# Performance work log

Measured on AMD Instinct MI355X. Metric: run time of the kernel, lower is better.

Reference implementation:

```python
import jax, jax.numpy as jnp
import numpy as np

N = 3072      # packed vision tokens (multiple of _BLOCK=128, so no padding needed)
D = 1280      # hidden_size
H = 16        # num_heads
K = 80        # head_dim = D // H
NSEG = 8      # number of packed images/segments


def setup_inputs() -> dict:
    key = jax.random.key(0)
    ks = jax.random.split(key, 8)
    hidden_ND = jax.random.normal(ks[0], (N, D), jnp.float32)
    inner = jnp.sort(jax.random.randint(ks[1], (NSEG - 1,), 1, N)).astype(jnp.int32)
    cu_seqlens = jnp.concatenate([
        jnp.zeros((1,), jnp.int32), inner, jnp.full((1,), N, jnp.int32)])
    theta = jax.random.uniform(ks[2], (N, K), jnp.float32, 0.0, 2.0 * np.pi)
    cos_NK = jnp.cos(theta)
    sin_NK = jnp.sin(theta)
    sd = 1.0 / np.sqrt(D)  # lecun_normal-ish scale
    qkv_w = jax.random.normal(ks[3], (D, 3 * D), jnp.float32) * sd
    qkv_b = jax.random.normal(ks[4], (3 * D,), jnp.float32) * 0.01
    proj_w = jax.random.normal(ks[5], (D, D), jnp.float32) * sd
    proj_b = jax.random.normal(ks[6], (D,), jnp.float32) * 0.01
    return {"hidden_ND": hidden_ND, "cu_seqlens": cu_seqlens,
            "cos_NK": cos_NK, "sin_NK": sin_NK,
            "qkv_w": qkv_w, "qkv_b": qkv_b,
            "proj_w": proj_w, "proj_b": proj_b}


def _rotate_half(x):
    x1, x2 = jnp.split(x, 2, axis=-1)
    return jnp.concatenate([-x2, x1], axis=-1)


def _apply_vision_rope(q_NHK, k_NHK, cos_NK, sin_NK):
    c = cos_NK[:, None, :]  # (N, 1, K) broadcast over heads
    s = sin_NK[:, None, :]
    q = q_NHK * c + _rotate_half(q_NHK) * s
    k = k_NHK * c + _rotate_half(k_NHK) * s
    return q, k


def reference(hidden_ND, cu_seqlens, cos_NK, sin_NK, qkv_w, qkv_b, proj_w, proj_b):
    n = hidden_ND.shape[0]
    scale = K ** (-0.5)
    qkv = (hidden_ND @ qkv_w + qkv_b).reshape(n, 3, H, K)
    q_NHK, k_NHK, v_NHK = qkv[:, 0], qkv[:, 1], qkv[:, 2]
    q_NHK, k_NHK = _apply_vision_rope(q_NHK, k_NHK, cos_NK, sin_NK)

    # segment-boundary mask: token i attends to [k_start[i], k_end[i])
    idx = jnp.arange(n)
    seg = jnp.searchsorted(cu_seqlens[1:], idx, side='right')
    nseg = cu_seqlens.shape[0]
    k_start = cu_seqlens[jnp.minimum(seg, nseg - 2)]
    k_end = cu_seqlens[jnp.minimum(seg + 1, nseg - 1)]
    mask = (idx[None, :] >= k_start[:, None]) & (idx[None, :] < k_end[:, None])  # (Nq, Nk)

    scores = jnp.einsum('nhk,mhk->hnm', q_NHK, k_NHK) * scale  # (H, N, N)
    scores = jnp.where(mask[None], scores, jnp.float32(-1e30))
    probs = jax.nn.softmax(scores, axis=-1)
    attn = jnp.einsum('hnm,mhk->nhk', probs, v_NHK)  # (N, H, K)
    out_ND = attn.reshape(n, H * K) @ proj_w + proj_b
    return out_ND
```

## Files before the change

kernel.cpp:

```cpp
#include <hip/hip_runtime.h>

#define NTOK 3072
#define DM   1280
#define NH   16
#define HD   80
#define HDP  96
#define NSEG 8
#define QKVC 3840

typedef __attribute__((ext_vector_type(4))) float  f32x4;
typedef __attribute__((ext_vector_type(8))) __bf16 bf16x8;
typedef __attribute__((ext_vector_type(8))) unsigned short ushort8;
typedef __attribute__((ext_vector_type(4))) unsigned short ushort4v;

static __device__ __forceinline__ unsigned short f2bf(float f){
  union{float f; unsigned int u;} v; v.f=f;
  unsigned int r = v.u + 0x7fffu + ((v.u>>16)&1u);
  return (unsigned short)(r>>16);
}
static __device__ __forceinline__ float bf2f(unsigned short u){
  union{unsigned int i; float f;} v; v.i = ((unsigned int)u)<<16; return v.f;
}
static __device__ __forceinline__ void gload_lds16(const void* g, void* l){
  __builtin_amdgcn_global_load_lds((const __attribute__((address_space(1))) void*)g,
                                   (__attribute__((address_space(3))) void*)l, 16, 0, 0);
}

__global__ void cast_f32_bf16(const float* __restrict__ src, unsigned short* __restrict__ dst, int n){
  int i = (blockIdx.x*256 + threadIdx.x)*4;
  if (i >= n) return;
  f32x4 v = *reinterpret_cast<const f32x4*>(&src[i]);
  ushort4v o;
  o[0]=f2bf(v[0]); o[1]=f2bf(v[1]); o[2]=f2bf(v[2]); o[3]=f2bf(v[3]);
  *reinterpret_cast<ushort4v*>(&dst[i]) = o;
}

__global__ void transpose_cast(const float* __restrict__ src, unsigned short* __restrict__ dst, int R, int C){
  __shared__ unsigned short tile[32][33];
  int c0 = blockIdx.x*32, r0 = blockIdx.y*32;
  int tx = threadIdx.x, ty = threadIdx.y;
  #pragma unroll
  for (int i=0;i<4;i++){
    int r = r0 + ty + i*8;
    tile[ty+i*8][tx] = f2bf(src[(size_t)r*C + c0 + tx]);
  }
  __syncthreads();
  #pragma unroll
  for (int i=0;i<4;i++){
    int c = c0 + ty + i*8;
    dst[(size_t)c*R + r0 + tx] = tile[tx][ty+i*8];
  }
}

template<int OUT_BF16>
__global__ __launch_bounds__(256) void gemm_bt(
    const unsigned short* __restrict__ A,
    const unsigned short* __restrict__ Bt,
    const float* __restrict__ bias,
    unsigned short* __restrict__ Cb,
    float* __restrict__ Cf,
    int M, int Ncol, int Kd)
{
  __shared__ unsigned short As[128*32];
  __shared__ unsigned short Bs[128*32];
  const int tid  = threadIdx.x;
  const int lane = tid & 63, wave = tid >> 6;
  const int wr = wave >> 1, wc = wave & 1;
  const int bm = blockIdx.y, bn = blockIdx.x;
  const f32x4 vzero = {0.f,0.f,0.f,0.f};

  f32x4 acc[4][4];
  #pragma unroll
  for (int i=0;i<4;i++)
    #pragma unroll
    for (int j=0;j<4;j++) acc[i][j] = vzero;

  const int rsub = lane>>2;
  const int kc   = (lane&3)*8;
  const unsigned short* Ab = A  + (size_t)(bm*128 + wave*32 + rsub)*Kd + kc;
  const unsigned short* Bb = Bt + (size_t)(bn*128 + wave*32 + rsub)*Kd + kc;

  for (int k0=0; k0<Kd; k0+=32){
    __syncthreads();
    #pragma unroll
    for (int i=0;i<2;i++){
      gload_lds16(Ab + (size_t)i*16*Kd + k0, &As[(wave*2+i)*512]);
      gload_lds16(Bb + (size_t)i*16*Kd + k0, &Bs[(wave*2+i)*512]);
    }
    __syncthreads();
    bf16x8 a[4], b[4];
    #pragma unroll
    for (int mf=0; mf<4; mf++)
      a[mf] = *reinterpret_cast<const bf16x8*>(&As[(wr*64 + mf*16 + (lane&15))*32 + ((lane>>4)<<3)]);
    #pragma unroll
    for (int nf=0; nf<4; nf++)
      b[nf] = *reinterpret_cast<const bf16x8*>(&Bs[(wc*64 + nf*16 + (lane&15))*32 + ((lane>>4)<<3)]);
    #pragma unroll
    for (int mf=0; mf<4; mf++)
      #pragma unroll
      for (int nf=0; nf<4; nf++)
        acc[mf][nf] = __builtin_amdgcn_mfma_f32_16x16x32_bf16(a[mf], b[nf], acc[mf][nf], 0,0,0);
  }

  const int crow0 = bm*128 + wr*64;
  const int ccol0 = bn*128 + wc*64;
  #pragma unroll
  for (int nf=0; nf<4; nf++){
    int col = ccol0 + nf*16 + (lane&15);
    float bv = bias[col];
    #pragma unroll
    for (int mf=0; mf<4; mf++){
      #pragma unroll
      for (int r=0;r<4;r++){
        int row = crow0 + mf*16 + ((lane>>4)<<2) + r;
        float v = acc[mf][nf][r] + bv;
        if (OUT_BF16) Cb[(size_t)row*Ncol + col] = f2bf(v);
        else          Cf[(size_t)row*Ncol + col] = v;
      }
    }
  }
}

__global__ void rope_repack(const unsigned short* __restrict__ qkv,
                            const float* __restrict__ cosNK, const float* __restrict__ sinNK,
                            unsigned short* __restrict__ Qr, unsigned short* __restrict__ Kr)
{
  int idx = blockIdx.x*256 + threadIdx.x;
  int k  = idx % HDP;
  int nh = idx / HDP;
  int n  = nh % NTOK;
  int h  = nh / NTOK;
  size_t dsti = (size_t)(h*NTOK + n)*HDP + k;
  if (k >= HD){ Qr[dsti]=0; Kr[dsti]=0; return; }
  float c = cosNK[n*HD + k], s = sinNK[n*HD + k];
  int   kp  = (k < 40) ? (k+40) : (k-40);
  float sgn = (k < 40) ? -1.f : 1.f;
  size_t base = (size_t)n*QKVC + h*HD;
  float q   = bf2f(qkv[base + k]);
  float qp  = bf2f(qkv[base + kp]);
  float kk  = bf2f(qkv[base + DM + k]);
  float kkp = bf2f(qkv[base + DM + kp]);
  Qr[dsti] = f2bf(q*c  + sgn*qp*s);
  Kr[dsti] = f2bf(kk*c + sgn*kkp*s);
}

__global__ __launch_bounds__(256) void attn_kernel(
    const unsigned short* __restrict__ Qr,
    const unsigned short* __restrict__ Kr,
    const unsigned short* __restrict__ qkv,
    const int* __restrict__ cu,
    unsigned short* __restrict__ attn_out)
{
  __shared__ unsigned short Qs[64*HDP];
  __shared__ unsigned short Ks[64*HDP];
  __shared__ unsigned short Vst[HDP*64];
  __shared__ unsigned short Ps[64*64];
  __shared__ int rs[64], re[64];

  const int h   = blockIdx.y;
  const int q0  = blockIdx.x*64;
  const int tid = threadIdx.x;
  const int lane = tid & 63;
  const int wave = tid >> 6;
  const f32x4 vzero = {0.f,0.f,0.f,0.f};

  if (tid < 64){
    int row = q0 + tid;
    int seg = 0;
    #pragma unroll
    for (int j=1;j<NSEG;j++) seg += (cu[j] <= row) ? 1 : 0;
    rs[tid] = cu[seg];
    re[tid] = cu[seg+1];
  }
  {
    const unsigned short* src = Qr + ((size_t)h*NTOK + q0)*HDP;
    #pragma unroll
    for (int i=0;i<3;i++){
      int off = i*2048 + tid*8;
      *reinterpret_cast<ushort8*>(&Qs[off]) = *reinterpret_cast<const ushort8*>(&src[off]);
    }
  }
  __syncthreads();
  int kmin = NTOK, kmax = 0;
  for (int j=0;j<64;j++){
    int a = rs[j]; if (a < kmin) kmin = a;
    int b = re[j]; if (b > kmax) kmax = b;
  }

  f32x4 accO[6];
  #pragma unroll
  for (int i=0;i<6;i++) accO[i] = vzero;
  float m_r[4] = {-1e30f,-1e30f,-1e30f,-1e30f};
  float l_r[4] = {0.f,0.f,0.f,0.f};
  const int row_lds0 = wave*16 + ((lane>>4)<<2);

  for (int kt = (kmin/64)*64; kt < kmax; kt += 64){
    __syncthreads();
    {
      const unsigned short* src = Kr + ((size_t)h*NTOK + kt)*HDP;
      #pragma unroll
      for (int i=0;i<3;i++){
        int off = i*2048 + tid*8;
        *reinterpret_cast<ushort8*>(&Ks[off]) = *reinterpret_cast<const ushort8*>(&src[off]);
      }
    }
    if (tid < 128){
      int r = tid >> 1, cb = (tid & 1)*40;
      const unsigned short* src = qkv + (size_t)(kt + r)*QKVC + 2*DM + h*HD + cb;
      #pragma unroll
      for (int jj=0;jj<5;jj++){
        ushort8 v = *reinterpret_cast<const ushort8*>(&src[jj*8]);
        #pragma unroll
        for (int e=0;e<8;e++) Vst[(cb + jj*8 + e)*64 + r] = v[e];
      }
    } else {
      int t2 = tid - 128;
      #pragma unroll
      for (int e=0;e<8;e++) Vst[80*64 + t2*8 + e] = 0;
    }
    __syncthreads();

    f32x4 accS[4];
    #pragma unroll
    for (int i=0;i<4;i++) accS[i] = vzero;
    #pragma unroll
    for (int ks=0; ks<3; ks++){
      bf16x8 aq = *reinterpret_cast<const bf16x8*>(&Qs[(wave*16 + (lane&15))*HDP + ks*32 + ((lane>>4)<<3)]);
      #pragma unroll
      for (int nf=0;nf<4;nf++){
        bf16x8 bk = *reinterpret_cast<const bf16x8*>(&Ks[(nf*16 + (lane&15))*HDP + ks*32 + ((lane>>4)<<3)]);
        accS[nf] = __builtin_amdgcn_mfma_f32_16x16x32_bf16(aq, bk, accS[nf], 0,0,0);
      }
    }
    const float scale = 0.11180339887498948f;
    #pragma unroll
    for (int r=0;r<4;r++){
      int row_i = row_lds0 + r;
      int rst = rs[row_i], ren = re[row_i];
      float sv[4]; bool ok[4];
      float mx = -1e30f;
      #pragma unroll
      for (int nf=0;nf<4;nf++){
        int kcol = kt + nf*16 + (lane&15);
        ok[nf] = (kcol >= rst) && (kcol < ren);
        sv[nf] = accS[nf][r]*scale;
        if (ok[nf]) mx = fmaxf(mx, sv[nf]);
      }
      #pragma unroll
      for (int d=1; d<16; d<<=1) mx = fmaxf(mx, __shfl_xor(mx, d, 64));
      float mnew  = fmaxf(m_r[r], mx);
      float alpha = __expf(m_r[r] - mnew);
      m_r[r] = mnew;
      float lsum = 0.f;
      #pragma unroll
      for (int nf=0;nf<4;nf++){
        float p = ok[nf] ? __expf(sv[nf] - mnew) : 0.f;
        Ps[row_i*64 + nf*16 + (lane&15)] = f2bf(p);
        lsum += p;
      }
      #pragma unroll
      for (int d=1; d<16; d<<=1) lsum += __shfl_xor(lsum, d, 64);
      l_r[r] = l_r[r]*alpha + lsum;
      #pragma unroll
      for (int cf=0; cf<6; cf++) accO[cf][r] *= alpha;
    }
    #pragma unroll
    for (int ks=0; ks<2; ks++){
      bf16x8 ap = *reinterpret_cast<const bf16x8*>(&Ps[(wave*16 + (lane&15))*64 + ks*32 + ((lane>>4)<<3)]);
      #pragma unroll
      for (int cf=0; cf<6; cf++){
        bf16x8 bv = *reinterpret_cast<const bf16x8*>(&Vst[(cf*16 + (lane&15))*64 + ks*32 + ((lane>>4)<<3)]);
        accO[cf] = __builtin_amdgcn_mfma_f32_16x16x32_bf16(ap, bv, accO[cf], 0,0,0);
      }
    }
  }

  #pragma unroll
  for (int cf=0; cf<5; cf++){
    #pragma unroll
    for (int r=0;r<4;r++){
      int row = q0 + row_lds0 + r;
      int col = h*HD + cf*16 + (lane&15);
      float o = accO[cf][r] / l_r[r];
      attn_out[(size_t)row*DM + col] = f2bf(o);
    }
  }
}

extern "C" void kernel_launch(void* const* d_in, const int* in_sizes, int n_in,
                              void* d_out, int out_size, void* d_ws, size_t ws_size,
                              hipStream_t stream)
{
  const float* hidden = (const float*)d_in[0];
  const int*   cu     = (const int*)  d_in[1];
  const float* cosNK  = (const float*)d_in[2];
  const float* sinNK  = (const float*)d_in[3];
  const float* qkv_w  = (const float*)d_in[4];
  const float* qkv_b  = (const float*)d_in[5];
  const float* proj_w = (const float*)d_in[6];
  const float* proj_b = (const float*)d_in[7];
  float* out = (float*)d_out;

  char* w = (char*)d_ws;
  unsigned short* hid_bf  = (unsigned short*)w;  w += (size_t)NTOK*DM*2;
  unsigned short* qkvwT   = (unsigned short*)w;  w += (size_t)QKVC*DM*2;
  unsigned short* projwT  = (unsigned short*)w;  w += (size_t)DM*DM*2;
  unsigned short* qkv_bf  = (unsigned short*)w;  w += (size_t)NTOK*QKVC*2;
  unsigned short* Qr      = (unsigned short*)w;  w += (size_t)NH*NTOK*HDP*2;
  unsigned short* Kr      = (unsigned short*)w;  w += (size_t)NH*NTOK*HDP*2;
  unsigned short* attn_bf = (unsigned short*)w;  w += (size_t)NTOK*DM*2;

  cast_f32_bf16<<<(NTOK*DM/4 + 255)/256, 256, 0, stream>>>(hidden, hid_bf, NTOK*DM);
  transpose_cast<<<dim3(QKVC/32, DM/32), dim3(32,8), 0, stream>>>(qkv_w, qkvwT, DM, QKVC);
  transpose_cast<<<dim3(DM/32,  DM/32), dim3(32,8), 0, stream>>>(proj_w, projwT, DM, DM);
  gemm_bt<1><<<dim3(QKVC/128, NTOK/128), 256, 0, stream>>>(hid_bf, qkvwT, qkv_b, qkv_bf, nullptr, NTOK, QKVC, DM);
  rope_repack<<<(NH*NTOK*HDP)/256, 256, 0, stream>>>(qkv_bf, cosNK, sinNK, Qr, Kr);
  attn_kernel<<<dim3(NTOK/64, NH), 256, 0, stream>>>(Qr, Kr, qkv_bf, cu, attn_bf);
  gemm_bt<0><<<dim3(DM/128, NTOK/128), 256, 0, stream>>>(attn_bf, projwT, proj_b, nullptr, out, NTOK, DM, DM);
}
```

Measured before the change: 266.4 us.

## Restructure attention with 128-wide KV tiles, pre-transposed V and async LDS loads

The attention kernel now processes 128 keys per iteration instead of 64. A new transpose_v kernel writes V once into a head-major, token-contiguous layout, which replaces the per-block scalar transpose into shared memory. Q, K and V tiles are loaded with global_load_lds. The K/Q row stride is padded to 104, and the P and V tiles use XOR swizzles to cut LDS bank conflicts; the padded fifth output fragment is also dropped. This trades an extra kernel launch and more LDS per block (which may lower occupancy) for fewer loop iterations, cheaper staging and less per-tile overhead.

```diff
diff --git a/kernel.cpp b/kernel.cpp
--- a/kernel.cpp
+++ b/kernel.cpp
@@ -4,7 +4,8 @@
 #define DM   1280
 #define NH   16
 #define HD   80
-#define HDP  96
+#define HDS  104
+#define KVB  128
 #define NSEG 8
 #define QKVC 3840
 
@@ -49,6 +50,24 @@
   for (int i=0;i<4;i++){
     int c = c0 + ty + i*8;
     dst[(size_t)c*R + r0 + tx] = tile[tx][ty+i*8];
+  }
+}
+
+__global__ void transpose_v(const unsigned short* __restrict__ qkv, unsigned short* __restrict__ Vt){
+  __shared__ unsigned short tile[32][33];
+  int n0 = blockIdx.x*32, d0 = blockIdx.y*32, h = blockIdx.z;
+  int tx = threadIdx.x, ty = threadIdx.y;
+  #pragma unroll
+  for (int i=0;i<4;i++){
+    int n = n0 + ty + i*8;
+    int d = d0 + tx;
+    tile[ty+i*8][tx] = (d < HD) ? qkv[(size_t)n*QKVC + 2*DM + h*HD + d] : (unsigned short)0;
+  }
+  __syncthreads();
+  #pragma unroll
+  for (int i=0;i<4;i++){
+    int d = d0 + ty + i*8;
+    if (d < HD) Vt[((size_t)h*HD + d)*NTOK + n0 + tx] = tile[tx][ty+i*8];
   }
 }
 
@@ -126,11 +145,12 @@
                             unsigned short* __restrict__ Qr, unsigned short* __restrict__ Kr)
 {
   int idx = blockIdx.x*256 + threadIdx.x;
-  int k  = idx % HDP;
-  int nh = idx / HDP;
+  if (idx >= NH*NTOK*HDS) return;
+  int k  = idx % HDS;
+  int nh = idx / HDS;
   int n  = nh % NTOK;
   int h  = nh / NTOK;
-  size_t dsti = (size_t)(h*NTOK + n)*HDP + k;
+  size_t dsti = (size_t)(h*NTOK + n)*HDS + k;
   if (k >= HD){ Qr[dsti]=0; Kr[dsti]=0; return; }
   float c = cosNK[n*HD + k], s = sinNK[n*HD + k];
   int   kp  = (k < 40) ? (k+40) : (k-40);
@@ -147,101 +167,90 @@
 __global__ __launch_bounds__(256) void attn_kernel(
     const unsigned short* __restrict__ Qr,
     const unsigned short* __restrict__ Kr,
-    const unsigned short* __restrict__ qkv,
+    const unsigned short* __restrict__ Vt,
     const int* __restrict__ cu,
     unsigned short* __restrict__ attn_out)
 {
-  __shared__ unsigned short Qs[64*HDP];
-  __shared__ unsigned short Ks[64*HDP];
-  __shared__ unsigned short Vst[HDP*64];
-  __shared__ unsigned short Ps[64*64];
+  __shared__ unsigned short Qs[64*HDS];
+  __shared__ unsigned short Ks[KVB*HDS];
+  __shared__ unsigned short Vs[HD*KVB];
+  __shared__ unsigned short Ps[64*KVB];
   __shared__ int rs[64], re[64];
 
   const int h   = blockIdx.y;
   const int q0  = blockIdx.x*64;
   const int tid = threadIdx.x;
-  const int lane = tid & 63;
-  const int wave = tid >> 6;
+  const int lane = tid & 63, wave = tid >> 6;
+  const int l16 = lane & 15, g16 = lane >> 4;
   const f32x4 vzero = {0.f,0.f,0.f,0.f};
 
   if (tid < 64){
-    int row = q0 + tid;
-    int seg = 0;
+    int row = q0 + tid, seg = 0;
     #pragma unroll
     for (int j=1;j<NSEG;j++) seg += (cu[j] <= row) ? 1 : 0;
-    rs[tid] = cu[seg];
-    re[tid] = cu[seg+1];
+    rs[tid] = cu[seg]; re[tid] = cu[seg+1];
   }
   {
-    const unsigned short* src = Qr + ((size_t)h*NTOK + q0)*HDP;
-    #pragma unroll
-    for (int i=0;i<3;i++){
-      int off = i*2048 + tid*8;
-      *reinterpret_cast<ushort8*>(&Qs[off]) = *reinterpret_cast<const ushort8*>(&src[off]);
+    const char* src = (const char*)(Qr + (size_t)(h*NTOK + q0)*HDS);
+    #pragma unroll
+    for (int i=0;i<4;i++){
+      int t = tid + i*256;
+      if (t < 832) gload_lds16(src + (size_t)t*16, (char*)Qs + (size_t)t*16);
     }
   }
   __syncthreads();
-  int kmin = NTOK, kmax = 0;
-  for (int j=0;j<64;j++){
-    int a = rs[j]; if (a < kmin) kmin = a;
-    int b = re[j]; if (b > kmax) kmax = b;
-  }
-
-  f32x4 accO[6];
-  #pragma unroll
-  for (int i=0;i<6;i++) accO[i] = vzero;
+  const int kmin = rs[0], kmax = re[63];
+
+  f32x4 accO[5];
+  #pragma unroll
+  for (int i=0;i<5;i++) accO[i] = vzero;
   float m_r[4] = {-1e30f,-1e30f,-1e30f,-1e30f};
   float l_r[4] = {0.f,0.f,0.f,0.f};
-  const int row_lds0 = wave*16 + ((lane>>4)<<2);
-
-  for (int kt = (kmin/64)*64; kt < kmax; kt += 64){
+  const float scale = 0.11180339887498948f;
+
+  for (int kt = (kmin/KVB)*KVB; kt < kmax; kt += KVB){
     __syncthreads();
     {
-      const unsigned short* src = Kr + ((size_t)h*NTOK + kt)*HDP;
-      #pragma unroll
-      for (int i=0;i<3;i++){
-        int off = i*2048 + tid*8;
-        *reinterpret_cast<ushort8*>(&Ks[off]) = *reinterpret_cast<const ushort8*>(&src[off]);
-      }
-    }
-    if (tid < 128){
-      int r = tid >> 1, cb = (tid & 1)*40;
-      const unsigned short* src = qkv + (size_t)(kt + r)*QKVC + 2*DM + h*HD + cb;
-      #pragma unroll
-      for (int jj=0;jj<5;jj++){
-        ushort8 v = *reinterpret_cast<const ushort8*>(&src[jj*8]);
-        #pragma unroll
-        for (int e=0;e<8;e++) Vst[(cb + jj*8 + e)*64 + r] = v[e];
-      }
-    } else {
-      int t2 = tid - 128;
-      #pragma unroll
-      for (int e=0;e<8;e++) Vst[80*64 + t2*8 + e] = 0;
+      const char* src = (const char*)(Kr + (size_t)(h*NTOK + kt)*HDS);
+      #pragma unroll
+      for (int i=0;i<7;i++){
+        int t = tid + i*256;
+        if (t < 1664) gload_lds16(src + (size_t)t*16, (char*)Ks + (size_t)t*16);
+      }
+    }
+    {
+      #pragma unroll
+      for (int i=0;i<5;i++){
+        int t = tid + i*256;
+        int row = t >> 4;
+        int ch  = (t & 15) ^ (row & 7);
+        const unsigned short* src = Vt + ((size_t)h*HD + row)*NTOK + kt + ch*8;
+        gload_lds16(src, (char*)Vs + (size_t)t*16);
+      }
     }
     __syncthreads();
 
-    f32x4 accS[4];
-    #pragma unroll
-    for (int i=0;i<4;i++) accS[i] = vzero;
+    f32x4 accS[8];
+    #pragma unroll
+    for (int i=0;i<8;i++) accS[i] = vzero;
     #pragma unroll
     for (int ks=0; ks<3; ks++){
-      bf16x8 aq = *reinterpret_cast<const bf16x8*>(&Qs[(wave*16 + (lane&15))*HDP + ks*32 + ((lane>>4)<<3)]);
-      #pragma unroll
-      for (int nf=0;nf<4;nf++){
-        bf16x8 bk = *reinterpret_cast<const bf16x8*>(&Ks[(nf*16 + (lane&15))*HDP + ks*32 + ((lane>>4)<<3)]);
+      bf16x8 aq = *reinterpret_cast<const bf16x8*>((const char*)Qs + (wave*16 + l16)*208 + ks*64 + g16*16);
+      #pragma unroll
+      for (int nf=0;nf<8;nf++){
+        bf16x8 bk = *reinterpret_cast<const bf16x8*>((const char*)Ks + (nf*16 + l16)*208 + ks*64 + g16*16);
         accS[nf] = __builtin_amdgcn_mfma_f32_16x16x32_bf16(aq, bk, accS[nf], 0,0,0);
       }
     }
-    const float scale = 0.11180339887498948f;
     #pragma unroll
     for (int r=0;r<4;r++){
-      int row_i = row_lds0 + r;
-      int rst = rs[row_i], ren = re[row_i];
-      float sv[4]; bool ok[4];
+      const int row_i = wave*16 + g16*4 + r;
+      const int rst = rs[row_i], ren = re[row_i];
+      float sv[8]; bool ok[8];
       float mx = -1e30f;
       #pragma unroll
-      for (int nf=0;nf<4;nf++){
-        int kcol = kt + nf*16 + (lane&15);
+      for (int nf=0;nf<8;nf++){
+        int kcol = kt + nf*16 + l16;
         ok[nf] = (kcol >= rst) && (kcol < ren);
         sv[nf] = accS[nf][r]*scale;
         if (ok[nf]) mx = fmaxf(mx, sv[nf]);
@@ -253,23 +262,26 @@
       m_r[r] = mnew;
       float lsum = 0.f;
       #pragma unroll
-      for (int nf=0;nf<4;nf++){
+      for (int nf=0;nf<8;nf++){
         float p = ok[nf] ? __expf(sv[nf] - mnew) : 0.f;
-        Ps[row_i*64 + nf*16 + (lane&15)] = f2bf(p);
+        int pb = (row_i*256 + nf*32 + l16*2) ^ ((row_i&7)<<4);
+        *reinterpret_cast<unsigned short*>((char*)Ps + pb) = f2bf(p);
         lsum += p;
       }
       #pragma unroll
       for (int d=1; d<16; d<<=1) lsum += __shfl_xor(lsum, d, 64);
       l_r[r] = l_r[r]*alpha + lsum;
       #pragma unroll
-      for (int cf=0; cf<6; cf++) accO[cf][r] *= alpha;
-    }
-    #pragma unroll
-    for (int ks=0; ks<2; ks++){
-      bf16x8 ap = *reinterpret_cast<const bf16x8*>(&Ps[(wave*16 + (lane&15))*64 + ks*32 + ((lane>>4)<<3)]);
-      #pragma unroll
-      for (int cf=0; cf<6; cf++){
-        bf16x8 bv = *reinterpret_cast<const bf16x8*>(&Vst[(cf*16 + (lane&15))*64 + ks*32 + ((lane>>4)<<3)]);
+      for (int cf=0; cf<5; cf++) accO[cf][r] *= alpha;
+    }
+    #pragma unroll
+    for (int ks=0; ks<4; ks++){
+      const int arow = wave*16 + l16;
+      bf16x8 ap = *reinterpret_cast<const bf16x8*>((char*)Ps + ((arow*256 + ks*64 + g16*16) ^ ((arow&7)<<4)));
+      #pragma unroll
+      for (int cf=0; cf<5; cf++){
+        const int vrow = cf*16 + l16;
+        bf16x8 bv = *reinterpret_cast<const bf16x8*>((char*)Vs + ((vrow*256 + ks*64 + g16*16) ^ ((vrow&7)<<4)));
         accO[cf] = __builtin_amdgcn_mfma_f32_16x16x32_bf16(ap, bv, accO[cf], 0,0,0);
       }
     }
@@ -279,10 +291,9 @@
   for (int cf=0; cf<5; cf++){
     #pragma unroll
     for (int r=0;r<4;r++){
-      int row = q0 + row_lds0 + r;
-      int col = h*HD + cf*16 + (lane&15);
-      float o = accO[cf][r] / l_r[r];
-      attn_out[(size_t)row*DM + col] = f2bf(o);
+      int row = q0 + wave*16 + g16*4 + r;
+      int col = h*HD + cf*16 + l16;
+      attn_out[(size_t)row*DM + col] = f2bf(accO[cf][r] / l_r[r]);
     }
   }
 }
@@ -306,15 +317,17 @@
   unsigned short* qkvwT   = (unsigned short*)w;  w += (size_t)QKVC*DM*2;
   unsigned short* projwT  = (unsigned short*)w;  w += (size_t)DM*DM*2;
   unsigned short* qkv_bf  = (unsigned short*)w;  w += (size_t)NTOK*QKVC*2;
-  unsigned short* Qr      = (unsigned short*)w;  w += (size_t)NH*NTOK*HDP*2;
-  unsigned short* Kr      = (unsigned short*)w;  w += (size_t)NH*NTOK*HDP*2;
-  unsigned short* attn_bf = (unsigned short*)w;  w += (size_t)NTOK*DM*2;
+  unsigned short* Qr      = (unsigned short*)w;  w += (size_t)NH*NTOK*HDS*2;
+  unsigned short* Kr      = (unsigned short*)w;  w += (size_t)NH*NTOK*HDS*2;
+  unsigned short* Vt      = qkvwT;
+  unsigned short* attn_bf = hid_bf;
 
   cast_f32_bf16<<<(NTOK*DM/4 + 255)/256, 256, 0, stream>>>(hidden, hid_bf, NTOK*DM);
   transpose_cast<<<dim3(QKVC/32, DM/32), dim3(32,8), 0, stream>>>(qkv_w, qkvwT, DM, QKVC);
   transpose_cast<<<dim3(DM/32,  DM/32), dim3(32,8), 0, stream>>>(proj_w, projwT, DM, DM);
   gemm_bt<1><<<dim3(QKVC/128, NTOK/128), 256, 0, stream>>>(hid_bf, qkvwT, qkv_b, qkv_bf, nullptr, NTOK, QKVC, DM);
-  rope_repack<<<(NH*NTOK*HDP)/256, 256, 0, stream>>>(qkv_bf, cosNK, sinNK, Qr, Kr);
-  attn_kernel<<<dim3(NTOK/64, NH), 256, 0, stream>>>(Qr, Kr, qkv_bf, cu, attn_bf);
+  rope_repack<<<(NH*NTOK*HDS + 255)/256, 256, 0, stream>>>(qkv_bf, cosNK, sinNK, Qr, Kr);
+  transpose_v<<<dim3(NTOK/32, 3, NH), dim3(32,8), 0, stream>>>(qkv_bf, Vt);
+  attn_kernel<<<dim3(NTOK/64, NH), 256, 0, stream>>>(Qr, Kr, Vt, cu, attn_bf);
   gemm_bt<0><<<dim3(DM/128, NTOK/128), 256, 0, stream>>>(attn_bf, projwT, proj_b, nullptr, out, NTOK, DM, DM);
 }
```

After: 273.2 us. 2.6% more time.
